# Kernel optimization log

Measured on AMD Instinct MI355X. Metric: run time of the kernel, lower is better.

The kernel has to match this reference:

```python
import jax, jax.numpy as jnp
import numpy as np


def setup_inputs() -> dict:
    key = jax.random.key(0)
    k1, k2, k3, k4, k5, k6 = jax.random.split(key, 6)
    B, N, C, H = 4096, 64, 192, 6
    NW = 64  # windows per image; must divide B
    TABLE = 225  # (2*8-1)**2
    qkv = jax.random.normal(k1, (B, N, 3 * C), dtype=jnp.float32)
    rpi = jax.random.randint(k2, (N, N), 0, TABLE, dtype=jnp.int64)
    mask = jax.random.normal(k3, (NW, N, N), dtype=jnp.float32)
    rpb_table = jax.random.normal(k4, (TABLE, H), dtype=jnp.float32) * 0.02
    proj_w = jax.random.normal(k5, (C, C), dtype=jnp.float32) * 0.02
    proj_b = jax.random.normal(k6, (C,), dtype=jnp.float32) * 0.02
    return {"qkv": qkv, "rpi": rpi, "mask": mask, "rpb_table": rpb_table,
            "proj_w": proj_w, "proj_b": proj_b}


def reference(qkv, rpi, mask, rpb_table, proj_w, proj_b):
    b_, n, c3 = qkv.shape
    c = c3 // 3
    h = rpb_table.shape[1]           # num_heads
    hd = c // h                      # head_dim
    scale = hd ** (-0.5)
    # (b_, n, 3, h, hd) -> (3, b_, h, n, hd)
    qkv = qkv.reshape(b_, n, 3, h, hd).transpose(2, 0, 3, 1, 4)
    q, k, v = qkv[0] * scale, qkv[1], qkv[2]
    # windowed QK^T: [b_, h, n, n]
    attn = jnp.einsum('bhqd,bhkd->bhqk', q, k)
    # relative position bias gather: rpi [n,n] -> [h,n,n]
    bias = rpb_table[rpi].transpose(2, 0, 1)
    attn = attn + bias[None]
    # shift-window mask add
    nw = mask.shape[0]
    attn = attn.reshape(b_ // nw, nw, h, n, n) + mask[None, :, None]
    attn = attn.reshape(b_, h, n, n)
    attn = jax.nn.softmax(attn, axis=-1)
    # AV then output projection
    out = jnp.einsum('bhqk,bhkd->bhqd', attn, v)
    out = out.transpose(0, 2, 1, 3).reshape(b_, n, c)
    return out @ proj_w.T + proj_b
```

## Files before the change

kernel.cpp:

```cpp
#include <hip/hip_runtime.h>
#include <stdint.h>

typedef __bf16 bf16x8 __attribute__((ext_vector_type(8)));
typedef float f32x4 __attribute__((ext_vector_type(4)));

__device__ __forceinline__ unsigned short f2bf(float f) {
    union { __bf16 h; unsigned short u; } v;
    v.h = (__bf16)f;
    return v.u;
}

#define QS_STRIDE 40
#define VT_STRIDE 72
#define PS_STRIDE 72
#define XS_STRIDE 200

__global__ void prep_all(const int* __restrict__ rpi32,
                         const float* __restrict__ mask,
                         const float* __restrict__ rpb,
                         const float* __restrict__ proj_w,
                         float* __restrict__ bm,
                         unsigned short* __restrict__ wf) {
    int bid = blockIdx.x;
    int tid = threadIdx.x;
    if (bid < 6144) {
        __shared__ int is64_s;
        if (tid == 0) {
            int s = 0;
            #pragma unroll
            for (int i = 0; i < 16; ++i) s |= rpi32[2 * i + 1];
            is64_s = (s == 0);
        }
        __syncthreads();
        int g = bid * 256 + tid;
        int wh = g >> 12;
        int e  = g & 4095;
        int c = e >> 6, r = e & 63;
        int h = wh % 6, w = wh / 6;
        int rc = r * 64 + c;
        int rv = is64_s ? rpi32[2 * rc] : rpi32[rc];
        bm[g] = mask[w * 4096 + rc] + rpb[rv * 6 + h];
    } else {
        int g = (bid - 6144) * 256 + tid;
        int e = g & 7;
        int lane = (g >> 3) & 63;
        int kkct = g >> 9;
        int kk = kkct / 12, ct = kkct % 12;
        int co = ct * 16 + (lane & 15);
        int ki = kk * 32 + (lane >> 4) * 8 + e;
        wf[g] = f2bf(proj_w[co * 192 + ki]);
    }
}


__global__ __launch_bounds__(256, 3)
void winattn_fast(const float* __restrict__ qkv,
                  const float* __restrict__ bm,
                  const unsigned short* __restrict__ wf,
                  const float* __restrict__ proj_b,
                  float* __restrict__ out) {
    __shared__ __align__(16) unsigned short x_s[64 * XS_STRIDE];
    __shared__ __align__(16) unsigned short u_s[7424];
    __shared__ __align__(16) unsigned short p_s[4 * 16 * PS_STRIDE];

    unsigned short* q_s  = u_s;
    unsigned short* k_s  = u_s + 2560;
    unsigned short* vT_s = u_s + 5120;

    const int tid  = threadIdx.x;
    const int b    = blockIdx.x;
    const int lane = tid & 63;
    const int wv   = tid >> 6;
    const int l16  = lane & 15;
    const int lhi  = lane >> 4;
    const int qbase = wv * 16;
    const float scale = 0.17677669529663687f;

    const float* qkv_b = qkv + (size_t)b * 64 * 576;
    const float* bm_w  = bm + (size_t)(b & 63) * 6 * 4096;

    const int tokA = tid >> 3;
    const int dA   = (tid & 7) << 2;
    const float4* gA = (const float4*)(qkv_b + tokA * 576 + dA);
    const float4* gB = (const float4*)(qkv_b + (tokA + 32) * 576 + dA);

    float4 q0, k0, v0, q1, k1, v1;

#define LOADH(h_)  do { int o = (h_) * 8;                         \
        q0 = gA[o];      k0 = gA[o + 48]; v0 = gA[o + 96];        \
        q1 = gB[o];      k1 = gB[o + 48]; v1 = gB[o + 96]; } while (0)

#define STOREH() do {                                             \
        ushort4 qh, kh;                                           \
        qh.x = f2bf(q0.x * scale); qh.y = f2bf(q0.y * scale);     \
        qh.z = f2bf(q0.z * scale); qh.w = f2bf(q0.w * scale);     \
        kh.x = f2bf(k0.x); kh.y = f2bf(k0.y);                     \
        kh.z = f2bf(k0.z); kh.w = f2bf(k0.w);                     \
        *(ushort4*)&q_s[tokA * QS_STRIDE + dA] = qh;              \
        *(ushort4*)&k_s[tokA * QS_STRIDE + dA] = kh;              \
        vT_s[(dA + 0) * VT_STRIDE + tokA] = f2bf(v0.x);           \
        vT_s[(dA + 1) * VT_STRIDE + tokA] = f2bf(v0.y);           \
        vT_s[(dA + 2) * VT_STRIDE + tokA] = f2bf(v0.z);           \
        vT_s[(dA + 3) * VT_STRIDE + tokA] = f2bf(v0.w);           \
        qh.x = f2bf(q1.x * scale); qh.y = f2bf(q1.y * scale);     \
        qh.z = f2bf(q1.z * scale); qh.w = f2bf(q1.w * scale);     \
        kh.x = f2bf(k1.x); kh.y = f2bf(k1.y);                     \
        kh.z = f2bf(k1.z); kh.w = f2bf(k1.w);                     \
        *(ushort4*)&q_s[(tokA + 32) * QS_STRIDE + dA] = qh;       \
        *(ushort4*)&k_s[(tokA + 32) * QS_STRIDE + dA] = kh;       \
        vT_s[(dA + 0) * VT_STRIDE + tokA + 32] = f2bf(v1.x);      \
        vT_s[(dA + 1) * VT_STRIDE + tokA + 32] = f2bf(v1.y);      \
        vT_s[(dA + 2) * VT_STRIDE + tokA + 32] = f2bf(v1.z);      \
        vT_s[(dA + 3) * VT_STRIDE + tokA + 32] = f2bf(v1.w); } while (0)

    LOADH(0);
    STOREH();

    unsigned short* pw = p_s + wv * 16 * PS_STRIDE;

    for (int h = 0; h < 6; ++h) {
        __syncthreads();
        if (h < 5) LOADH(h + 1);

        const float* bmh = bm_w + h * 4096;
        float4 bv[4];
        #pragma unroll
        for (int nt = 0; nt < 4; ++nt)
            bv[nt] = *(const float4*)&bmh[(nt * 16 + l16) * 64 + qbase + lhi * 4];

        bf16x8 aq = *(const bf16x8*)&q_s[(qbase + l16) * QS_STRIDE + lhi * 8];
        float lg[4][4];
        #pragma unroll
        for (int nt = 0; nt < 4; ++nt) {
            bf16x8 bk = *(const bf16x8*)&k_s[(nt * 16 + l16) * QS_STRIDE + lhi * 8];
            f32x4 c = {0.f, 0.f, 0.f, 0.f};
            c = __builtin_amdgcn_mfma_f32_16x16x32_bf16(aq, bk, c, 0, 0, 0);
            lg[nt][0] = c[0] + bv[nt].x; lg[nt][1] = c[1] + bv[nt].y;
            lg[nt][2] = c[2] + bv[nt].z; lg[nt][3] = c[3] + bv[nt].w;
        }

        float srow[4];
        float p[4][4];
        #pragma unroll
        for (int j = 0; j < 4; ++j) {
            float m = fmaxf(fmaxf(lg[0][j], lg[1][j]), fmaxf(lg[2][j], lg[3][j]));
            #pragma unroll
            for (int o = 1; o < 16; o <<= 1) m = fmaxf(m, __shfl_xor(m, o, 64));
            float s = 0.f;
            #pragma unroll
            for (int nt = 0; nt < 4; ++nt) { p[nt][j] = __expf(lg[nt][j] - m); s += p[nt][j]; }
            #pragma unroll
            for (int o = 1; o < 16; o <<= 1) s += __shfl_xor(s, o, 64);
            srow[j] = s;
        }

        #pragma unroll
        for (int nt = 0; nt < 4; ++nt)
            #pragma unroll
            for (int j = 0; j < 4; ++j)
                pw[(lhi * 4 + j) * PS_STRIDE + nt * 16 + l16] = f2bf(p[nt][j]);

        f32x4 xo[2] = {{0.f,0.f,0.f,0.f},{0.f,0.f,0.f,0.f}};
        #pragma unroll
        for (int kk = 0; kk < 2; ++kk) {
            bf16x8 pa = *(const bf16x8*)&pw[l16 * PS_STRIDE + kk * 32 + lhi * 8];
            #pragma unroll
            for (int dt = 0; dt < 2; ++dt) {
                bf16x8 vb = *(const bf16x8*)&vT_s[(dt * 16 + l16) * VT_STRIDE + kk * 32 + lhi * 8];
                xo[dt] = __builtin_amdgcn_mfma_f32_16x16x32_bf16(pa, vb, xo[dt], 0, 0, 0);
            }
        }
        #pragma unroll
        for (int j = 0; j < 4; ++j) {
            float inv = __builtin_amdgcn_rcpf(srow[j]);
            int n = qbase + lhi * 4 + j;
            #pragma unroll
            for (int dt = 0; dt < 2; ++dt)
                x_s[n * XS_STRIDE + h * 32 + dt * 16 + l16] = f2bf(xo[dt][j] * inv);
        }

        __syncthreads();
        if (h < 5) STOREH();
    }
#undef LOADH
#undef STOREH

    f32x4 oacc[12];
    #pragma unroll
    for (int ct = 0; ct < 12; ++ct) oacc[ct] = (f32x4){0.f, 0.f, 0.f, 0.f};
    #pragma unroll
    for (int kk = 0; kk < 6; ++kk) {
        bf16x8 ax = *(const bf16x8*)&x_s[(qbase + l16) * XS_STRIDE + kk * 32 + lhi * 8];
        #pragma unroll
        for (int ct = 0; ct < 12; ++ct) {
            bf16x8 bw = *(const bf16x8*)&wf[((kk * 12 + ct) * 64 + lane) * 8];
            oacc[ct] = __builtin_amdgcn_mfma_f32_16x16x32_bf16(ax, bw, oacc[ct], 0, 0, 0);
        }
    }
    float* outb = out + (size_t)b * 64 * 192;
    #pragma unroll
    for (int ct = 0; ct < 12; ++ct) {
        int co = ct * 16 + l16;
        float bias = proj_b[co];
        #pragma unroll
        for (int j = 0; j < 4; ++j) {
            int n = qbase + lhi * 4 + j;
            outb[n * 192 + co] = oacc[ct][j] + bias;
        }
    }
}


#define WS_STRIDE 40

__global__ __launch_bounds__(256)
void winattn_fused(const float* __restrict__ qkv,
                   const int* __restrict__ rpi32,
                   const float* __restrict__ mask,
                   const float* __restrict__ rpb_table,
                   const float* __restrict__ proj_w,
                   const float* __restrict__ proj_b,
                   float* __restrict__ out) {
    __shared__ __align__(16) unsigned short x_s[64 * XS_STRIDE];
    __shared__ __align__(16) unsigned short u_s[12032];
    __shared__ float rpb_s[225];
    __shared__ int rpi_is64_s;

    unsigned short* q_s  = u_s;
    unsigned short* k_s  = u_s + 2560;
    unsigned short* vT_s = u_s + 5120;
    unsigned short* p_s  = u_s + 7424;
    unsigned short* w_s  = u_s;

    const int tid  = threadIdx.x;
    const int b    = blockIdx.x;
    const int lane = tid & 63;
    const int wv   = tid >> 6;
    const int l16  = lane & 15;
    const int lhi  = lane >> 4;
    const int qbase = wv * 16;
    const float scale = 0.17677669529663687f;

    if (tid == 0) {
        int s = 0;
        #pragma unroll
        for (int i = 0; i < 16; ++i) s |= rpi32[2 * i + 1];
        rpi_is64_s = (s == 0) ? 1 : 0;
    }

    const float* maskw = mask + (size_t)(b & 63) * 4096;
    const float* qkv_b = qkv + (size_t)b * 64 * 576;

    for (int h = 0; h < 6; ++h) {
        for (int idx = tid; idx < 64 * 8; idx += 256) {
            int tok = idx >> 3, d = (idx & 7) << 2;
            const float4* base = (const float4*)(qkv_b + tok * 576 + h * 32 + d);
            float4 qv = base[0];
            float4 kv = base[48];
            float4 vv = base[96];
            ushort4 qh, kh;
            qh.x = f2bf(qv.x * scale); qh.y = f2bf(qv.y * scale);
            qh.z = f2bf(qv.z * scale); qh.w = f2bf(qv.w * scale);
            kh.x = f2bf(kv.x); kh.y = f2bf(kv.y); kh.z = f2bf(kv.z); kh.w = f2bf(kv.w);
            *(ushort4*)&q_s[tok * QS_STRIDE + d] = qh;
            *(ushort4*)&k_s[tok * QS_STRIDE + d] = kh;
            vT_s[(d + 0) * VT_STRIDE + tok] = f2bf(vv.x);
            vT_s[(d + 1) * VT_STRIDE + tok] = f2bf(vv.y);
            vT_s[(d + 2) * VT_STRIDE + tok] = f2bf(vv.z);
            vT_s[(d + 3) * VT_STRIDE + tok] = f2bf(vv.w);
        }
        if (tid < 225) rpb_s[tid] = rpb_table[tid * 6 + h];
        __syncthreads();
        const int is64 = rpi_is64_s;

        bf16x8 aq = *(const bf16x8*)&q_s[(qbase + l16) * QS_STRIDE + lhi * 8];
        float lg[4][4];
        #pragma unroll
        for (int nt = 0; nt < 4; ++nt) {
            bf16x8 bk = *(const bf16x8*)&k_s[(nt * 16 + l16) * QS_STRIDE + lhi * 8];
            f32x4 c = {0.f, 0.f, 0.f, 0.f};
            c = __builtin_amdgcn_mfma_f32_16x16x32_bf16(aq, bk, c, 0, 0, 0);
            #pragma unroll
            for (int j = 0; j < 4; ++j) lg[nt][j] = c[j];
        }
        #pragma unroll
        for (int nt = 0; nt < 4; ++nt) {
            int c = nt * 16 + l16;
            #pragma unroll
            for (int j = 0; j < 4; ++j) {
                int r = qbase + lhi * 4 + j;
                int e = r * 64 + c;
                int rv = is64 ? rpi32[2 * e] : rpi32[e];
                lg[nt][j] += rpb_s[rv] + maskw[e];
            }
        }
        float srow[4];
        float p[4][4];
        #pragma unroll
        for (int j = 0; j < 4; ++j) {
            float m = fmaxf(fmaxf(lg[0][j], lg[1][j]), fmaxf(lg[2][j], lg[3][j]));
            #pragma unroll
            for (int o = 1; o < 16; o <<= 1) m = fmaxf(m, __shfl_xor(m, o, 64));
            float s = 0.f;
            #pragma unroll
            for (int nt = 0; nt < 4; ++nt) { p[nt][j] = __expf(lg[nt][j] - m); s += p[nt][j]; }
            #pragma unroll
            for (int o = 1; o < 16; o <<= 1) s += __shfl_xor(s, o, 64);
            srow[j] = s;
        }
        __syncthreads();
        unsigned short* pw = p_s + wv * 16 * PS_STRIDE;
        #pragma unroll
        for (int nt = 0; nt < 4; ++nt)
            #pragma unroll
            for (int j = 0; j < 4; ++j)
                pw[(lhi * 4 + j) * PS_STRIDE + nt * 16 + l16] = f2bf(p[nt][j]);
        __syncthreads();

        f32x4 xo[2] = {{0.f,0.f,0.f,0.f},{0.f,0.f,0.f,0.f}};
        #pragma unroll
        for (int kk = 0; kk < 2; ++kk) {
            bf16x8 pa = *(const bf16x8*)&pw[l16 * PS_STRIDE + kk * 32 + lhi * 8];
            #pragma unroll
            for (int dt = 0; dt < 2; ++dt) {
                bf16x8 vb = *(const bf16x8*)&vT_s[(dt * 16 + l16) * VT_STRIDE + kk * 32 + lhi * 8];
                xo[dt] = __builtin_amdgcn_mfma_f32_16x16x32_bf16(pa, vb, xo[dt], 0, 0, 0);
            }
        }
        #pragma unroll
        for (int j = 0; j < 4; ++j) {
            float inv = 1.f / srow[j];
            int n = qbase + lhi * 4 + j;
            #pragma unroll
            for (int dt = 0; dt < 2; ++dt)
                x_s[n * XS_STRIDE + h * 32 + dt * 16 + l16] = f2bf(xo[dt][j] * inv);
        }
        __syncthreads();
    }

    f32x4 oacc[12];
    #pragma unroll
    for (int ct = 0; ct < 12; ++ct) oacc[ct] = (f32x4){0.f, 0.f, 0.f, 0.f};
    for (int kk = 0; kk < 6; ++kk) {
        for (int idx = tid; idx < 192 * 8; idx += 256) {
            int co = idx >> 3, d = (idx & 7) << 2;
            float4 wvv = *(const float4*)(proj_w + co * 192 + kk * 32 + d);
            ushort4 wh;
            wh.x = f2bf(wvv.x); wh.y = f2bf(wvv.y); wh.z = f2bf(wvv.z); wh.w = f2bf(wvv.w);
            *(ushort4*)&w_s[co * WS_STRIDE + d] = wh;
        }
        __syncthreads();
        bf16x8 ax = *(const bf16x8*)&x_s[(qbase + l16) * XS_STRIDE + kk * 32 + lhi * 8];
        #pragma unroll
        for (int ct = 0; ct < 12; ++ct) {
            bf16x8 bw = *(const bf16x8*)&w_s[(ct * 16 + l16) * WS_STRIDE + lhi * 8];
            oacc[ct] = __builtin_amdgcn_mfma_f32_16x16x32_bf16(ax, bw, oacc[ct], 0, 0, 0);
        }
        __syncthreads();
    }
    float* outb = out + (size_t)b * 64 * 192;
    #pragma unroll
    for (int ct = 0; ct < 12; ++ct) {
        int co = ct * 16 + l16;
        float bias = proj_b[co];
        #pragma unroll
        for (int j = 0; j < 4; ++j) {
            int n = qbase + lhi * 4 + j;
            outb[n * 192 + co] = oacc[ct][j] + bias;
        }
    }
}

extern "C" void kernel_launch(void* const* d_in, const int* in_sizes, int n_in,
                              void* d_out, int out_size, void* d_ws, size_t ws_size,
                              hipStream_t stream) {
    (void)in_sizes; (void)n_in; (void)out_size;
    const float* qkv       = (const float*)d_in[0];
    const int*   rpi       = (const int*)d_in[1];
    const float* mask      = (const float*)d_in[2];
    const float* rpb_table = (const float*)d_in[3];
    const float* proj_w    = (const float*)d_in[4];
    const float* proj_b    = (const float*)d_in[5];
    float* out = (float*)d_out;

    const size_t BM_BYTES = (size_t)64 * 6 * 4096 * sizeof(float);
    const size_t WF_BYTES = (size_t)36864 * sizeof(unsigned short);

    if (ws_size >= BM_BYTES + WF_BYTES) {
        float* bmp = (float*)d_ws;
        unsigned short* wfp = (unsigned short*)((char*)d_ws + BM_BYTES);
        prep_all<<<6144 + 144, 256, 0, stream>>>(rpi, mask, rpb_table, proj_w, bmp, wfp);
        winattn_fast<<<4096, 256, 0, stream>>>(qkv, bmp, wfp, proj_b, out);
    } else {
        winattn_fused<<<4096, 256, 0, stream>>>(qkv, rpi, mask, rpb_table, proj_w, proj_b, out);
    }
}
```

Before: 212.5 us.

## Transpose QK^T MFMA output so softmax rows reduce in-lane with vector P stores

Swaps the MFMA operands so each lane holds logits for a single query row across keys. The row max and sum now mostly reduce inside the lane and need only two cross-lane shuffles instead of four per row. Normalization moves before the P store, which becomes a packed ushort4 write. The bias/mask precompute layout is transposed to row-major to match, which also makes that prep kernel's reads contiguous. The cost is normalizing 16 values per lane before PV instead of 8 after it.

Result: faster. 192.9 us (-9.2%).

```diff
diff --git a/kernel.cpp b/kernel.cpp
--- a/kernel.cpp
+++ b/kernel.cpp
@@ -35,11 +35,9 @@
         int g = bid * 256 + tid;
         int wh = g >> 12;
         int e  = g & 4095;
-        int c = e >> 6, r = e & 63;
         int h = wh % 6, w = wh / 6;
-        int rc = r * 64 + c;
-        int rv = is64_s ? rpi32[2 * rc] : rpi32[rc];
-        bm[g] = mask[w * 4096 + rc] + rpb[rv * 6 + h];
+        int rv = is64_s ? rpi32[2 * e] : rpi32[e];
+        bm[g] = mask[w * 4096 + e] + rpb[rv * 6 + h];
     } else {
         int g = (bid - 6144) * 256 + tid;
         int e = g & 7;
@@ -126,7 +124,7 @@
         float4 bv[4];
         #pragma unroll
         for (int nt = 0; nt < 4; ++nt)
-            bv[nt] = *(const float4*)&bmh[(nt * 16 + l16) * 64 + qbase + lhi * 4];
+            bv[nt] = *(const float4*)&bmh[(qbase + l16) * 64 + nt * 16 + lhi * 4];
 
         bf16x8 aq = *(const bf16x8*)&q_s[(qbase + l16) * QS_STRIDE + lhi * 8];
         float lg[4][4];
@@ -134,31 +132,34 @@
         for (int nt = 0; nt < 4; ++nt) {
             bf16x8 bk = *(const bf16x8*)&k_s[(nt * 16 + l16) * QS_STRIDE + lhi * 8];
             f32x4 c = {0.f, 0.f, 0.f, 0.f};
-            c = __builtin_amdgcn_mfma_f32_16x16x32_bf16(aq, bk, c, 0, 0, 0);
+            c = __builtin_amdgcn_mfma_f32_16x16x32_bf16(bk, aq, c, 0, 0, 0);
             lg[nt][0] = c[0] + bv[nt].x; lg[nt][1] = c[1] + bv[nt].y;
             lg[nt][2] = c[2] + bv[nt].z; lg[nt][3] = c[3] + bv[nt].w;
         }
 
-        float srow[4];
-        float p[4][4];
-        #pragma unroll
-        for (int j = 0; j < 4; ++j) {
-            float m = fmaxf(fmaxf(lg[0][j], lg[1][j]), fmaxf(lg[2][j], lg[3][j]));
-            #pragma unroll
-            for (int o = 1; o < 16; o <<= 1) m = fmaxf(m, __shfl_xor(m, o, 64));
-            float s = 0.f;
-            #pragma unroll
-            for (int nt = 0; nt < 4; ++nt) { p[nt][j] = __expf(lg[nt][j] - m); s += p[nt][j]; }
-            #pragma unroll
-            for (int o = 1; o < 16; o <<= 1) s += __shfl_xor(s, o, 64);
-            srow[j] = s;
-        }
-
+        float m = lg[0][0];
         #pragma unroll
         for (int nt = 0; nt < 4; ++nt)
             #pragma unroll
-            for (int j = 0; j < 4; ++j)
-                pw[(lhi * 4 + j) * PS_STRIDE + nt * 16 + l16] = f2bf(p[nt][j]);
+            for (int j = 0; j < 4; ++j) m = fmaxf(m, lg[nt][j]);
+        m = fmaxf(m, __shfl_xor(m, 16, 64));
+        m = fmaxf(m, __shfl_xor(m, 32, 64));
+        float s = 0.f;
+        #pragma unroll
+        for (int nt = 0; nt < 4; ++nt)
+            #pragma unroll
+            for (int j = 0; j < 4; ++j) { lg[nt][j] = __expf(lg[nt][j] - m); s += lg[nt][j]; }
+        s += __shfl_xor(s, 16, 64);
+        s += __shfl_xor(s, 32, 64);
+        float inv = __builtin_amdgcn_rcpf(s);
+
+        #pragma unroll
+        for (int nt = 0; nt < 4; ++nt) {
+            ushort4 ph;
+            ph.x = f2bf(lg[nt][0] * inv); ph.y = f2bf(lg[nt][1] * inv);
+            ph.z = f2bf(lg[nt][2] * inv); ph.w = f2bf(lg[nt][3] * inv);
+            *(ushort4*)&pw[l16 * PS_STRIDE + nt * 16 + lhi * 4] = ph;
+        }
 
         f32x4 xo[2] = {{0.f,0.f,0.f,0.f},{0.f,0.f,0.f,0.f}};
         #pragma unroll
@@ -172,11 +173,10 @@
         }
         #pragma unroll
         for (int j = 0; j < 4; ++j) {
-            float inv = __builtin_amdgcn_rcpf(srow[j]);
             int n = qbase + lhi * 4 + j;
             #pragma unroll
             for (int dt = 0; dt < 2; ++dt)
-                x_s[n * XS_STRIDE + h * 32 + dt * 16 + l16] = f2bf(xo[dt][j] * inv);
+                x_s[n * XS_STRIDE + h * 32 + dt * 16 + l16] = f2bf(xo[dt][j]);
         }
 
         __syncthreads();
```
